# Kernel tuning notes

Measured on AMD Instinct MI355X. Metric: run time of the kernel, lower is better.

Reference implementation:

```python
import jax, jax.numpy as jnp
import numpy as np

N_NODES = 100000
N_EDGES = 1600000
D_IN = 128
D_HID = 128
D_OUT = 1


def setup_inputs() -> dict:
    key = jax.random.key(0)
    ks = jax.random.split(key, 8)
    x = jax.random.normal(ks[0], (N_NODES, D_IN), dtype=jnp.float32)
    edge_index = jax.random.randint(ks[1], (2, N_EDGES), 0, N_NODES, dtype=jnp.int64)
    s1 = 1.0 / np.sqrt(D_IN)
    s2 = 1.0 / np.sqrt(D_HID)
    W1 = jax.random.uniform(ks[2], (D_IN, D_HID), jnp.float32, -s1, s1)
    b1 = jnp.zeros((D_HID,), jnp.float32)
    W2 = jax.random.uniform(ks[3], (D_HID, D_HID), jnp.float32, -s2, s2)
    b2 = jnp.zeros((D_HID,), jnp.float32)
    Wl = jax.random.uniform(ks[4], (D_HID, D_OUT), jnp.float32, -s2, s2)
    bl = jax.random.uniform(ks[5], (D_OUT,), jnp.float32, -s2, s2)
    return {"x": x, "edge_index": edge_index, "W1": W1, "b1": b1,
            "W2": W2, "b2": b2, "Wl": Wl, "bl": bl}


def _gcn_norm(edge_index, num_nodes):
    # Add self-loops, compute symmetric normalization 1/sqrt(deg_s * deg_d).
    loops = jnp.arange(num_nodes, dtype=edge_index.dtype)
    src = jnp.concatenate([edge_index[0], loops])
    dst = jnp.concatenate([edge_index[1], loops])
    deg = jax.ops.segment_sum(jnp.ones_like(dst, dtype=jnp.float32), dst,
                              num_segments=num_nodes)
    dinv = jnp.where(deg > 0, jax.lax.rsqrt(deg), 0.0)
    norm = dinv[src] * dinv[dst]  # [E + N]
    return src, dst, norm


def _gcn_conv(h, W, b, src, dst, norm, num_nodes):
    h = h @ W                                  # [N, d_out]
    msg = h[src] * norm[:, None]               # [E+N, d_out] gather
    out = jax.ops.segment_sum(msg, dst, num_segments=num_nodes)  # scatter-add
    return out + b


def reference(x, edge_index, W1, b1, W2, b2, Wl, bl):
    num_nodes = x.shape[0]
    src, dst, norm = _gcn_norm(edge_index, num_nodes)
    h = jax.nn.relu(_gcn_conv(x, W1, b1, src, dst, norm, num_nodes))
    # dropout is identity in eval mode
    h = jax.nn.relu(_gcn_conv(h, W2, b2, src, dst, norm, num_nodes))
    return h @ Wl + bl
```

## Files before the change

### kernel.cpp

```cpp
#include <hip/hip_runtime.h>

#define DHID 128
#define BCAP 10240
#define PCHUNK 4096
#define XS_LD 136

typedef _Float16 h4 __attribute__((ext_vector_type(4)));
typedef _Float16 h8 __attribute__((ext_vector_type(8)));
typedef _Float16 f16x8 __attribute__((ext_vector_type(8)));
typedef float    f32x4 __attribute__((ext_vector_type(4)));

__global__ __launch_bounds__(256) void k_partition(const int* __restrict__ ei, int E, int nbuck,
                                                   int* __restrict__ bucket_cursor,
                                                   unsigned* __restrict__ packed) {
    __shared__ unsigned sdata[PCHUNK];
    __shared__ int lcnt[256], lbase[256], loff[256], lcur[256], sscan[256];
    int t = threadIdx.x;
    int e0 = blockIdx.x * PCHUNK;
    lcnt[t] = 0;
    __syncthreads();

    for (int i = t; i < PCHUNK; i += 256) {
        int e = e0 + i;
        if (e < E) {
            int d = ei[E + e];
            atomicAdd(&lcnt[d >> 9], 1);
        }
    }
    __syncthreads();

    int c = lcnt[t];
    sscan[t] = c;
    __syncthreads();
    for (int off = 1; off < 256; off <<= 1) {
        int v = (t >= off) ? sscan[t - off] : 0;
        __syncthreads();
        sscan[t] += v;
        __syncthreads();
    }
    loff[t] = sscan[t] - c;
    if (t < nbuck && c > 0) lbase[t] = atomicAdd(&bucket_cursor[t], c);
    lcur[t] = sscan[t] - c;
    __syncthreads();

    for (int i = t; i < PCHUNK; i += 256) {
        int e = e0 + i;
        if (e < E) {
            int s = ei[e];
            int d = ei[E + e];
            int b = d >> 9;
            int pos = atomicAdd(&lcur[b], 1);
            sdata[pos] = ((unsigned)(d & 511) << 17) | (unsigned)s;
        }
    }
    __syncthreads();

    int wid = t >> 6, lane = t & 63;
    for (int b = wid; b < nbuck; b += 4) {
        int cb = lcnt[b];
        if (cb == 0) continue;
        int gbase = b * BCAP + lbase[b];
        int sbase = loff[b];
        for (int k = lane; k < cb; k += 64) packed[gbase + k] = sdata[sbase + k];
    }
}

__global__ __launch_bounds__(256) void k_p2a(const unsigned* __restrict__ packed,
                                             const int* __restrict__ bucket_cursor,
                                             int* __restrict__ cnt,
                                             float* __restrict__ dinv, int N) {
    __shared__ int c512[512];
    int t = threadIdx.x, b = blockIdx.x;
    c512[t] = 0; c512[t + 256] = 0;
    __syncthreads();
    int m = bucket_cursor[b];
    const unsigned* pb = packed + (size_t)b * BCAP;
    for (int i = t; i < m; i += 256) atomicAdd(&c512[pb[i] >> 17], 1);
    __syncthreads();
    int base = b << 9;
#pragma unroll
    for (int j = 0; j < 2; ++j) {
        int node = base + t + j * 256;
        if (node < N) {
            int c = c512[t + j * 256];
            cnt[node] = c;
            dinv[node] = rsqrtf((float)(c + 1));
        }
    }
}

__global__ void k_reduce(const int* __restrict__ cnt, int* __restrict__ partial, int N) {
    __shared__ int s[256];
    int t = threadIdx.x;
    int i = blockIdx.x * 256 + t;
    s[t] = (i < N) ? cnt[i] : 0;
    __syncthreads();
    for (int st = 128; st > 0; st >>= 1) {
        if (t < st) s[t] += s[t + st];
        __syncthreads();
    }
    if (t == 0) partial[blockIdx.x] = s[0];
}

__global__ void k_scan_partials(const int* __restrict__ partial, int* __restrict__ blockoff, int NB) {
    __shared__ int s[1024];
    int t = threadIdx.x;
    s[t] = (t < NB) ? partial[t] : 0;
    __syncthreads();
    for (int off = 1; off < 1024; off <<= 1) {
        int v = (t >= off) ? s[t - off] : 0;
        __syncthreads();
        s[t] += v;
        __syncthreads();
    }
    if (t < NB) blockoff[t] = (t == 0) ? 0 : s[t - 1];
}

__global__ void k_scan_block(const int* __restrict__ cnt, const int* __restrict__ blockoff,
                             int* __restrict__ row_ptr, int N, int E) {
    __shared__ int s[256];
    int t = threadIdx.x;
    int i = blockIdx.x * 256 + t;
    int c = (i < N) ? cnt[i] : 0;
    s[t] = c;
    __syncthreads();
    for (int off = 1; off < 256; off <<= 1) {
        int v = (t >= off) ? s[t - off] : 0;
        __syncthreads();
        s[t] += v;
        __syncthreads();
    }
    if (i < N) row_ptr[i] = blockoff[blockIdx.x] + s[t] - c;
    if (i == 0) row_ptr[N] = E;
}

__global__ __launch_bounds__(256) void k_p2b(const unsigned* __restrict__ packed,
                                             const int* __restrict__ bucket_cursor,
                                             const int* __restrict__ row_ptr,
                                             int* __restrict__ csr, int N) {
    __shared__ int c512[512], cur512[512], sscan[256];
    int t = threadIdx.x, b = blockIdx.x;
    c512[t] = 0; c512[t + 256] = 0;
    __syncthreads();
    int m = bucket_cursor[b];
    const unsigned* pb = packed + (size_t)b * BCAP;
    for (int i = t; i < m; i += 256) atomicAdd(&c512[pb[i] >> 17], 1);
    __syncthreads();
    int v0 = c512[2 * t], v1 = c512[2 * t + 1];
    int ps = v0 + v1;
    sscan[t] = ps;
    __syncthreads();
    for (int off = 1; off < 256; off <<= 1) {
        int v = (t >= off) ? sscan[t - off] : 0;
        __syncthreads();
        sscan[t] += v;
        __syncthreads();
    }
    int excl = sscan[t] - ps;
    cur512[2 * t] = excl;
    cur512[2 * t + 1] = excl + v0;
    __syncthreads();
    int rbase = row_ptr[b << 9];
    for (int i = t; i < m; i += 256) {
        unsigned p = pb[i];
        int dl = p >> 17;
        int src = (int)(p & 0x1FFFFu);
        int pos = atomicAdd(&cur512[dl], 1);
        csr[rbase + pos] = src;
    }
}

template <typename TIN>
__global__ __launch_bounds__(256) void k_gemm_mfma(const TIN* __restrict__ X,
                                                   const float* __restrict__ W,
                                                   const float* __restrict__ dinv,
                                                   _Float16* __restrict__ Th, int N) {
    __shared__ _Float16 Xs[64 * XS_LD];
    int t = threadIdx.x;
    int w = t >> 6;
    int l = t & 63;
    int l16 = l & 15;
    int lq = l >> 4;

    f16x8 afrag[2][4];
#pragma unroll
    for (int ct = 0; ct < 2; ++ct) {
        int c = w * 32 + ct * 16 + l16;
#pragma unroll
        for (int kb = 0; kb < 4; ++kb) {
            f16x8 a;
#pragma unroll
            for (int j = 0; j < 8; ++j)
                a[j] = (_Float16)W[(kb * 32 + lq * 8 + j) * DHID + c];
            afrag[ct][kb] = a;
        }
    }

    int rs = t >> 2;
    int cs = (t & 3) * 32;

    int r0 = blockIdx.x * 64;
    {
        int rg = r0 + rs; if (rg > N - 1) rg = N - 1;
        _Float16* sp = Xs + rs * XS_LD + cs;
        if constexpr (sizeof(TIN) == 4) {
            const float* xp = (const float*)X + (size_t)rg * DHID + cs;
#pragma unroll
            for (int k = 0; k < 4; ++k) {
                float4 a = *(const float4*)(xp + k * 8);
                float4 b = *(const float4*)(xp + k * 8 + 4);
                h8 v;
                v[0] = (_Float16)a.x; v[1] = (_Float16)a.y;
                v[2] = (_Float16)a.z; v[3] = (_Float16)a.w;
                v[4] = (_Float16)b.x; v[5] = (_Float16)b.y;
                v[6] = (_Float16)b.z; v[7] = (_Float16)b.w;
                *(h8*)(sp + k * 8) = v;
            }
        } else {
            const _Float16* xp = (const _Float16*)X + (size_t)rg * DHID + cs;
#pragma unroll
            for (int k = 0; k < 4; ++k)
                *(h8*)(sp + k * 8) = *(const h8*)(xp + k * 8);
        }
    }
    __syncthreads();

    f32x4 acc[4][2];
#pragma unroll
    for (int rt = 0; rt < 4; ++rt)
#pragma unroll
        for (int ct = 0; ct < 2; ++ct) acc[rt][ct] = (f32x4){0.f, 0.f, 0.f, 0.f};

#pragma unroll
    for (int rt = 0; rt < 4; ++rt) {
        const _Float16* bp = Xs + (rt * 16 + l16) * XS_LD + lq * 8;
#pragma unroll
        for (int kb = 0; kb < 4; ++kb) {
            f16x8 b = *(const f16x8*)(bp + kb * 32);
            acc[rt][0] = __builtin_amdgcn_mfma_f32_16x16x32_f16(afrag[0][kb], b, acc[rt][0], 0, 0, 0);
            acc[rt][1] = __builtin_amdgcn_mfma_f32_16x16x32_f16(afrag[1][kb], b, acc[rt][1], 0, 0, 0);
        }
    }

#pragma unroll
    for (int rt = 0; rt < 4; ++rt) {
        int r = r0 + rt * 16 + l16;
        if (r < N) {
            float s = dinv[r];
#pragma unroll
            for (int ct = 0; ct < 2; ++ct) {
                h4 v;
#pragma unroll
                for (int j = 0; j < 4; ++j) v[j] = (_Float16)(acc[rt][ct][j] * s);
                *(h4*)(Th + (size_t)r * DHID + w * 32 + ct * 16 + lq * 4) = v;
            }
        }
    }
}

template <int FINAL>
__global__ __launch_bounds__(256) void k_agg(const _Float16* __restrict__ Th,
                                             const int* __restrict__ row_ptr,
                                             const int* __restrict__ csr_src,
                                             const float* __restrict__ dinv,
                                             const float* __restrict__ bias,
                                             void* __restrict__ outp,
                                             const float* __restrict__ Wl,
                                             const float* __restrict__ bl, int N) {
    int node = blockIdx.x * 16 + (threadIdx.x >> 4);
    int sl = threadIdx.x & 15;
    if (node >= N) return;

    int e = row_ptr[node];
    int end = row_ptr[node + 1];
    const h8* Tl = (const h8*)Th + sl;

    float acc[8];
#pragma unroll
    for (int c = 0; c < 8; ++c) acc[c] = 0.f;

    for (; e + 4 <= end; e += 4) {
        int s0 = csr_src[e];
        int s1 = csr_src[e + 1];
        int s2 = csr_src[e + 2];
        int s3 = csr_src[e + 3];
        h8 v0 = Tl[(size_t)s0 * 16];
        h8 v1 = Tl[(size_t)s1 * 16];
        h8 v2 = Tl[(size_t)s2 * 16];
        h8 v3 = Tl[(size_t)s3 * 16];
#pragma unroll
        for (int c = 0; c < 8; ++c)
            acc[c] += ((float)v0[c] + (float)v1[c]) + ((float)v2[c] + (float)v3[c]);
    }
    for (; e < end; ++e) {
        int s0 = csr_src[e];
        h8 va = Tl[(size_t)s0 * 16];
#pragma unroll
        for (int c = 0; c < 8; ++c) acc[c] += (float)va[c];
    }

    {
        h8 tv = Tl[(size_t)node * 16];
#pragma unroll
        for (int c = 0; c < 8; ++c) acc[c] += (float)tv[c];
    }

    float dn = dinv[node];
    const float* bp = bias + sl * 8;
    float4 b0 = *(const float4*)bp;
    float4 b1 = *(const float4*)(bp + 4);
    float r[8];
    r[0] = fmaxf(fmaf(dn, acc[0], b0.x), 0.f);
    r[1] = fmaxf(fmaf(dn, acc[1], b0.y), 0.f);
    r[2] = fmaxf(fmaf(dn, acc[2], b0.z), 0.f);
    r[3] = fmaxf(fmaf(dn, acc[3], b0.w), 0.f);
    r[4] = fmaxf(fmaf(dn, acc[4], b1.x), 0.f);
    r[5] = fmaxf(fmaf(dn, acc[5], b1.y), 0.f);
    r[6] = fmaxf(fmaf(dn, acc[6], b1.z), 0.f);
    r[7] = fmaxf(fmaf(dn, acc[7], b1.w), 0.f);

    if (FINAL == 0) {
        h8 v;
#pragma unroll
        for (int c = 0; c < 8; ++c) v[c] = (_Float16)r[c];
        *(h8*)((_Float16*)outp + (size_t)node * DHID + sl * 8) = v;
    } else {
        const float* wp = Wl + sl * 8;
        float4 w0 = *(const float4*)wp;
        float4 w1 = *(const float4*)(wp + 4);
        float p = r[0] * w0.x + r[1] * w0.y + r[2] * w0.z + r[3] * w0.w +
                  r[4] * w1.x + r[5] * w1.y + r[6] * w1.z + r[7] * w1.w;
#pragma unroll
        for (int off = 8; off > 0; off >>= 1) p += __shfl_down(p, off, 16);
        if (sl == 0) ((float*)outp)[node] = p + bl[0];
    }
}

extern "C" void kernel_launch(void* const* d_in, const int* in_sizes, int n_in,
                              void* d_out, int out_size, void* d_ws, size_t ws_size,
                              hipStream_t stream) {
    const float* x  = (const float*)d_in[0];
    const int*   ei = (const int*)d_in[1];
    const float* W1 = (const float*)d_in[2];
    const float* b1 = (const float*)d_in[3];
    const float* W2 = (const float*)d_in[4];
    const float* b2 = (const float*)d_in[5];
    const float* Wl = (const float*)d_in[6];
    const float* bl = (const float*)d_in[7];
    float* out = (float*)d_out;

    int N = in_sizes[0] / DHID;
    int E = in_sizes[1] / 2;
    int NB = (N + 255) / 256;
    int nbuck = (N + 511) / 512;
    int nRB = (N + 63) / 64;

    char* ws = (char*)d_ws;
    size_t off = 0;
    auto alloc = [&](size_t bytes) -> void* {
        void* p = ws + off;
        off += (bytes + 255) & ~(size_t)255;
        return p;
    };
    int*      cnt      = (int*)alloc((size_t)N * 4);
    float*    dinv     = (float*)alloc((size_t)N * 4);
    int*      row_ptr  = (int*)alloc((size_t)(N + 1) * 4);
    int*      partial  = (int*)alloc((size_t)NB * 4);
    int*      blockoff = (int*)alloc((size_t)NB * 4);
    int*      bcur     = (int*)alloc((size_t)nbuck * 4);
    int*      csr      = (int*)alloc((size_t)E * 4);
    unsigned* packed   = (unsigned*)alloc((size_t)nbuck * BCAP * 4);
    _Float16* Th       = (_Float16*)alloc((size_t)N * DHID * 2);
    _Float16* H        = (_Float16*)alloc((size_t)N * DHID * 2);

    (void)hipMemsetAsync(bcur, 0, (size_t)nbuck * 4, stream);
    k_partition<<<(E + PCHUNK - 1) / PCHUNK, 256, 0, stream>>>(ei, E, nbuck, bcur, packed);
    k_p2a<<<nbuck, 256, 0, stream>>>(packed, bcur, cnt, dinv, N);
    k_reduce<<<NB, 256, 0, stream>>>(cnt, partial, N);
    k_scan_partials<<<1, 1024, 0, stream>>>(partial, blockoff, NB);
    k_scan_block<<<NB, 256, 0, stream>>>(cnt, blockoff, row_ptr, N, E);
    k_p2b<<<nbuck, 256, 0, stream>>>(packed, bcur, row_ptr, csr, N);

    k_gemm_mfma<float><<<nRB, 256, 0, stream>>>(x, W1, dinv, Th, N);
    k_agg<0><<<(N + 15) / 16, 256, 0, stream>>>(Th, row_ptr, csr, dinv, b1, H, nullptr, nullptr, N);

    k_gemm_mfma<_Float16><<<nRB, 256, 0, stream>>>(H, W2, dinv, Th, N);
    k_agg<1><<<(N + 15) / 16, 256, 0, stream>>>(Th, row_ptr, csr, dinv, b2, out, Wl, bl, N);
}
```

Before: 229.8 us.

## Derive CSR offsets from bucket scan and fold degree pass into p2b

The per-node count pass, the three-kernel node-level scan and the separate dinv computation are replaced by a single-block scan over bucket totals. k_p2b now writes row_ptr and dinv directly from its local per-bucket histogram. This removes four launches and one full read of the packed edge buffer. The partition kernel also keeps each thread's 16 edges in registers so the edge list is read from global memory once instead of twice. The bucket scan runs in one 256-thread block, so it assumes at most 256 buckets, which holds for 100k nodes (196 buckets).

```diff
diff --git a/kernel.cpp b/kernel.cpp
--- a/kernel.cpp
+++ b/kernel.cpp
@@ -20,13 +20,21 @@
     lcnt[t] = 0;
     __syncthreads();
 
-    for (int i = t; i < PCHUNK; i += 256) {
-        int e = e0 + i;
+    int sreg[16], dreg[16];
+#pragma unroll
+    for (int k = 0; k < 16; ++k) {
+        int e = e0 + t + k * 256;
         if (e < E) {
-            int d = ei[E + e];
-            atomicAdd(&lcnt[d >> 9], 1);
-        }
-    }
+            sreg[k] = ei[e];
+            dreg[k] = ei[E + e];
+        } else {
+            dreg[k] = -1;
+        }
+    }
+
+#pragma unroll
+    for (int k = 0; k < 16; ++k)
+        if (dreg[k] >= 0) atomicAdd(&lcnt[dreg[k] >> 9], 1);
     __syncthreads();
 
     int c = lcnt[t];
@@ -43,14 +51,12 @@
     lcur[t] = sscan[t] - c;
     __syncthreads();
 
-    for (int i = t; i < PCHUNK; i += 256) {
-        int e = e0 + i;
-        if (e < E) {
-            int s = ei[e];
-            int d = ei[E + e];
-            int b = d >> 9;
+#pragma unroll
+    for (int k = 0; k < 16; ++k) {
+        if (dreg[k] >= 0) {
+            int b = dreg[k] >> 9;
             int pos = atomicAdd(&lcur[b], 1);
-            sdata[pos] = ((unsigned)(d & 511) << 17) | (unsigned)s;
+            sdata[pos] = ((unsigned)(dreg[k] & 511) << 17) | (unsigned)sreg[k];
         }
     }
     __syncthreads();
@@ -65,63 +71,11 @@
     }
 }
 
-__global__ __launch_bounds__(256) void k_p2a(const unsigned* __restrict__ packed,
-                                             const int* __restrict__ bucket_cursor,
-                                             int* __restrict__ cnt,
-                                             float* __restrict__ dinv, int N) {
-    __shared__ int c512[512];
-    int t = threadIdx.x, b = blockIdx.x;
-    c512[t] = 0; c512[t + 256] = 0;
-    __syncthreads();
-    int m = bucket_cursor[b];
-    const unsigned* pb = packed + (size_t)b * BCAP;
-    for (int i = t; i < m; i += 256) atomicAdd(&c512[pb[i] >> 17], 1);
-    __syncthreads();
-    int base = b << 9;
-#pragma unroll
-    for (int j = 0; j < 2; ++j) {
-        int node = base + t + j * 256;
-        if (node < N) {
-            int c = c512[t + j * 256];
-            cnt[node] = c;
-            dinv[node] = rsqrtf((float)(c + 1));
-        }
-    }
-}
-
-__global__ void k_reduce(const int* __restrict__ cnt, int* __restrict__ partial, int N) {
+__global__ void k_bscan(const int* __restrict__ bcur, int* __restrict__ bbase,
+                        int* __restrict__ row_ptr, int nbuck, int N, int E) {
     __shared__ int s[256];
     int t = threadIdx.x;
-    int i = blockIdx.x * 256 + t;
-    s[t] = (i < N) ? cnt[i] : 0;
-    __syncthreads();
-    for (int st = 128; st > 0; st >>= 1) {
-        if (t < st) s[t] += s[t + st];
-        __syncthreads();
-    }
-    if (t == 0) partial[blockIdx.x] = s[0];
-}
-
-__global__ void k_scan_partials(const int* __restrict__ partial, int* __restrict__ blockoff, int NB) {
-    __shared__ int s[1024];
-    int t = threadIdx.x;
-    s[t] = (t < NB) ? partial[t] : 0;
-    __syncthreads();
-    for (int off = 1; off < 1024; off <<= 1) {
-        int v = (t >= off) ? s[t - off] : 0;
-        __syncthreads();
-        s[t] += v;
-        __syncthreads();
-    }
-    if (t < NB) blockoff[t] = (t == 0) ? 0 : s[t - 1];
-}
-
-__global__ void k_scan_block(const int* __restrict__ cnt, const int* __restrict__ blockoff,
-                             int* __restrict__ row_ptr, int N, int E) {
-    __shared__ int s[256];
-    int t = threadIdx.x;
-    int i = blockIdx.x * 256 + t;
-    int c = (i < N) ? cnt[i] : 0;
+    int c = (t < nbuck) ? bcur[t] : 0;
     s[t] = c;
     __syncthreads();
     for (int off = 1; off < 256; off <<= 1) {
@@ -130,13 +84,15 @@
         s[t] += v;
         __syncthreads();
     }
-    if (i < N) row_ptr[i] = blockoff[blockIdx.x] + s[t] - c;
-    if (i == 0) row_ptr[N] = E;
+    if (t <= nbuck) bbase[t] = (t == 0) ? 0 : s[t - 1];
+    if (t == 0) row_ptr[N] = E;
 }
 
 __global__ __launch_bounds__(256) void k_p2b(const unsigned* __restrict__ packed,
                                              const int* __restrict__ bucket_cursor,
-                                             const int* __restrict__ row_ptr,
+                                             const int* __restrict__ bbase,
+                                             int* __restrict__ row_ptr,
+                                             float* __restrict__ dinv,
                                              int* __restrict__ csr, int N) {
     __shared__ int c512[512], cur512[512], sscan[256];
     int t = threadIdx.x, b = blockIdx.x;
@@ -159,8 +115,19 @@
     int excl = sscan[t] - ps;
     cur512[2 * t] = excl;
     cur512[2 * t + 1] = excl + v0;
-    __syncthreads();
-    int rbase = row_ptr[b << 9];
+
+    int rbase = bbase[b];
+    int n0 = (b << 9) + 2 * t;
+    if (n0 < N) {
+        row_ptr[n0] = rbase + excl;
+        dinv[n0] = rsqrtf((float)(v0 + 1));
+    }
+    if (n0 + 1 < N) {
+        row_ptr[n0 + 1] = rbase + excl + v0;
+        dinv[n0 + 1] = rsqrtf((float)(v1 + 1));
+    }
+    __syncthreads();
+
     for (int i = t; i < m; i += 256) {
         unsigned p = pb[i];
         int dl = p >> 17;
@@ -351,7 +318,6 @@
 
     int N = in_sizes[0] / DHID;
     int E = in_sizes[1] / 2;
-    int NB = (N + 255) / 256;
     int nbuck = (N + 511) / 512;
     int nRB = (N + 63) / 64;
 
@@ -362,12 +328,10 @@
         off += (bytes + 255) & ~(size_t)255;
         return p;
     };
-    int*      cnt      = (int*)alloc((size_t)N * 4);
     float*    dinv     = (float*)alloc((size_t)N * 4);
     int*      row_ptr  = (int*)alloc((size_t)(N + 1) * 4);
-    int*      partial  = (int*)alloc((size_t)NB * 4);
-    int*      blockoff = (int*)alloc((size_t)NB * 4);
     int*      bcur     = (int*)alloc((size_t)nbuck * 4);
+    int*      bbase    = (int*)alloc((size_t)(nbuck + 1) * 4);
     int*      csr      = (int*)alloc((size_t)E * 4);
     unsigned* packed   = (unsigned*)alloc((size_t)nbuck * BCAP * 4);
     _Float16* Th       = (_Float16*)alloc((size_t)N * DHID * 2);
@@ -375,11 +339,8 @@
 
     (void)hipMemsetAsync(bcur, 0, (size_t)nbuck * 4, stream);
     k_partition<<<(E + PCHUNK - 1) / PCHUNK, 256, 0, stream>>>(ei, E, nbuck, bcur, packed);
-    k_p2a<<<nbuck, 256, 0, stream>>>(packed, bcur, cnt, dinv, N);
-    k_reduce<<<NB, 256, 0, stream>>>(cnt, partial, N);
-    k_scan_partials<<<1, 1024, 0, stream>>>(partial, blockoff, NB);
-    k_scan_block<<<NB, 256, 0, stream>>>(cnt, blockoff, row_ptr, N, E);
-    k_p2b<<<nbuck, 256, 0, stream>>>(packed, bcur, row_ptr, csr, N);
+    k_bscan<<<1, 256, 0, stream>>>(bcur, bbase, row_ptr, nbuck, N, E);
+    k_p2b<<<nbuck, 256, 0, stream>>>(packed, bcur, bbase, row_ptr, dinv, csr, N);
 
     k_gemm_mfma<float><<<nRB, 256, 0, stream>>>(x, W1, dinv, Th, N);
     k_agg<0><<<(N + 15) / 16, 256, 0, stream>>>(Th, row_ptr, csr, dinv, b1, H, nullptr, nullptr, N);
```

Result: faster. 214.1 us (-6.8%).
